# Kernel optimization log

Measured on AMD Instinct MI355X. Metric: run time of the kernel, lower is better.

Reference implementation:

```python
import jax, jax.numpy as jnp
import numpy as np

NUM_HEADS = 16
HIDDEN = 1024
HEAD_DIM = HIDDEN // NUM_HEADS


def setup_inputs() -> dict:
    key = jax.random.key(0)
    ks = jax.random.split(key, 8)
    B, S = 4, 1024
    scale = 0.02
    return {
        "hidden_states": jax.random.normal(ks[0], (B, S, HIDDEN), jnp.float32),
        "attention_mask": jnp.zeros((B, 1, 1, S), jnp.float32),
        "Wq": jax.random.normal(ks[1], (HIDDEN, HIDDEN), jnp.float32) * scale,
        "bq": jnp.zeros((HIDDEN,), jnp.float32),
        "Wk": jax.random.normal(ks[2], (HIDDEN, HIDDEN), jnp.float32) * scale,
        "bk": jnp.zeros((HIDDEN,), jnp.float32),
        "Wv": jax.random.normal(ks[3], (HIDDEN, HIDDEN), jnp.float32) * scale,
        "bv": jnp.zeros((HIDDEN,), jnp.float32),
    }


def _split_heads(x):
    # [B,S,H] -> [B,heads,S,head_dim]
    B, S, _ = x.shape
    return x.reshape(B, S, NUM_HEADS, HEAD_DIM).transpose(0, 2, 1, 3)


def reference(hidden_states, attention_mask, Wq, bq, Wk, bk, Wv, bv):
    # torch.nn.Linear convention: y = x @ W.T + b
    q = _split_heads(hidden_states @ Wq.T + bq)
    k = _split_heads(hidden_states @ Wk.T + bk)
    v = _split_heads(hidden_states @ Wv.T + bv)
    scores = jnp.einsum('bhqd,bhkd->bhqk', q, k) * (HEAD_DIM ** -0.5)
    scores = scores + attention_mask  # broadcast [B,1,1,S]
    probs = jax.nn.softmax(scores, axis=-1)
    context = jnp.einsum('bhqk,bhkd->bhqd', probs, v)  # [B,heads,S,head_dim]
    B, _, S, _ = context.shape
    return context.transpose(0, 2, 1, 3).reshape(B, S, HIDDEN)
```

## Files before the change

### kernel.cpp

```cpp
#include <hip/hip_runtime.h>
#include <hip/hip_bf16.h>
#include <stdint.h>

#define NH 16
#define HID 1024
#define HD 64
#define NB 4
#define SS 1024
#define MTOT (NB*SS)

typedef __attribute__((ext_vector_type(8))) short bf16x8;
typedef __attribute__((ext_vector_type(4))) float f32x4;
typedef __attribute__((ext_vector_type(16))) float f32x16;

#define LOG2E 1.44269504088896f

__device__ __forceinline__ unsigned short f2bf(float f) {
  union { float f; unsigned u; } v; v.f = f;
  unsigned u = v.u;
  return (unsigned short)((u + 0x7FFFu + ((u >> 16) & 1u)) >> 16);
}

__device__ __forceinline__ unsigned cvtpk(float lo, float hi) {
  unsigned r;
  asm("v_cvt_pk_bf16_f32 %0, %1, %2" : "=v"(r) : "v"(lo), "v"(hi));
  return r;
}

__device__ __forceinline__ void pl32swap(unsigned &a, unsigned &b) {
  asm("v_permlane32_swap_b32 %0, %1" : "+v"(a), "+v"(b));
}

__device__ __forceinline__ float exp2fast(float x) {
  float r;
  asm("v_exp_f32 %0, %1" : "=v"(r) : "v"(x));
  return r;
}

__device__ __forceinline__ void async16(void* lds, const void* g) {
  __builtin_amdgcn_global_load_lds(
      (const __attribute__((address_space(1))) unsigned*)g,
      (__attribute__((address_space(3))) unsigned*)lds, 16, 0, 0);
}

__global__ void cvt_all(const float4* __restrict__ X,
                        const float4* __restrict__ Wq,
                        const float4* __restrict__ Wk,
                        const float4* __restrict__ Wv,
                        ushort4* __restrict__ Xb,
                        ushort4* __restrict__ Wb) {
  int i = blockIdx.x * 256 + threadIdx.x;
  const float4* src; ushort4* dst; int idx;
  if (i < (MTOT * HID / 4)) {
    src = X; dst = Xb; idx = i;
  } else {
    int j = i - (MTOT * HID / 4);
    int sel = j >> 18;
    idx = j & 262143;
    src = (sel == 0) ? Wq : (sel == 1) ? Wk : Wv;
    dst = Wb + (size_t)sel * 262144;
  }
  float4 v = src[idx];
  ushort4 o;
  o.x = f2bf(v.x); o.y = f2bf(v.y); o.z = f2bf(v.z); o.w = f2bf(v.w);
  dst[idx] = o;
}

__global__ __launch_bounds__(256) void qkv_gemm(
    const ushort* __restrict__ Xb,
    const ushort* __restrict__ Wb,
    const float* __restrict__ bq,
    const float* __restrict__ bk,
    const float* __restrict__ bv,
    ushort* __restrict__ Q,
    ushort* __restrict__ K,
    ushort* __restrict__ Vt)
{
  __shared__ __attribute__((aligned(16))) ushort Al[3][128 * 32];
  __shared__ __attribute__((aligned(16))) ushort Bl[3][128 * 32];

  int bid = blockIdx.x;
  int swz = (bid & 7) * 96 + (bid >> 3);
  const int nbn = 3072 / 128;
  int bm = swz / nbn, bn = swz % nbn;
  int m0 = bm * 128, n0 = bn * 128;

  int tid = threadIdx.x;
  int wave = tid >> 6, lane = tid & 63;
  int g = lane >> 4, c = lane & 15;
  int wr = wave >> 1, wc = wave & 1;

  int srow = tid >> 2;
  int schunk = tid & 3;
  int ssw = (srow >> 1) & 3;
  const ushort* Asrc0 = Xb + (size_t)(m0 + srow) * 1024 + ((schunk ^ ssw) << 3);
  const ushort* Asrc1 = Xb + (size_t)(m0 + 64 + srow) * 1024 + ((schunk ^ ssw) << 3);
  const ushort* Bsrc0 = Wb + (size_t)(n0 + srow) * 1024 + ((schunk ^ ssw) << 3);
  const ushort* Bsrc1 = Wb + (size_t)(n0 + 64 + srow) * 1024 + ((schunk ^ ssw) << 3);
  int soff = srow * 64 + schunk * 16;

#define GSTAGE(bi) do {                                   \
    char* la_ = (char*)Al[bi]; char* lb_ = (char*)Bl[bi]; \
    async16(la_ + soff,        Asrc0);                    \
    async16(la_ + 4096 + soff, Asrc1);                    \
    async16(lb_ + soff,        Bsrc0);                    \
    async16(lb_ + 4096 + soff, Bsrc1);                    \
    Asrc0 += 32; Asrc1 += 32; Bsrc0 += 32; Bsrc1 += 32;   \
  } while (0)

  f32x4 acc[4][4] = {};
  int rsw = (c >> 1) & 3;
  int ch = ((g ^ rsw) << 4);

  GSTAGE(0);
  GSTAGE(1);

  int cur = 0, nxt = 2;
  for (int ks = 0; ks < 32; ++ks) {
    if (ks < 31) {
      asm volatile("s_waitcnt vmcnt(4)" ::: "memory");
    } else {
      asm volatile("s_waitcnt vmcnt(0)" ::: "memory");
    }
    __builtin_amdgcn_sched_barrier(0);
    __builtin_amdgcn_s_barrier();
    __builtin_amdgcn_sched_barrier(0);
    if (ks < 30) GSTAGE(nxt);

    const char* la = (const char*)Al[cur];
    const char* lb = (const char*)Bl[cur];
    bf16x8 a[4], b[4];
    #pragma unroll
    for (int m = 0; m < 4; ++m)
      a[m] = *(const bf16x8*)(la + (wr * 64 + m * 16 + c) * 64 + ch);
    #pragma unroll
    for (int n = 0; n < 4; ++n)
      b[n] = *(const bf16x8*)(lb + (wc * 64 + n * 16 + c) * 64 + ch);
    __builtin_amdgcn_s_setprio(1);
    #pragma unroll
    for (int m = 0; m < 4; ++m)
      #pragma unroll
      for (int n = 0; n < 4; ++n)
        acc[m][n] = __builtin_amdgcn_mfma_f32_16x16x32_bf16(a[m], b[n], acc[m][n], 0, 0, 0);
    __builtin_amdgcn_s_setprio(0);

    cur = (cur == 2) ? 0 : cur + 1;
    nxt = (nxt == 2) ? 0 : nxt + 1;
  }
#undef GSTAGE

  int sel = n0 >> 10;
  const float* bp = (sel == 0) ? bq : (sel == 1) ? bk : bv;
  float scl = (sel == 0) ? 0.125f * LOG2E : 1.0f;

  #pragma unroll
  for (int n = 0; n < 4; ++n) {
    int nn = (n0 & 1023) + wc * 64 + n * 16 + c;
    float bias = bp[nn];
    int h = nn >> 6, d = nn & 63;
    #pragma unroll
    for (int m = 0; m < 4; ++m) {
      int rowg = m0 + wr * 64 + m * 16 + g * 4;
      int bb = rowg >> 10;
      int s = rowg & 1023;
      #pragma unroll
      for (int r = 0; r < 4; ++r) {
        float val = (acc[m][n][r] + bias) * scl;
        unsigned short ob = f2bf(val);
        if (sel == 0)
          Q[(size_t)((bb * 16 + h) * 1024 + s + r) * 64 + d] = ob;
        else if (sel == 1)
          K[(size_t)((bb * 16 + h) * 1024 + s + r) * 64 + d] = ob;
        else
          Vt[(size_t)((bb * 16 + h) * 64 + d) * 1024 + s + r] = ob;
      }
    }
  }
}

__device__ __forceinline__ void build_pa(const f32x16& p, bf16x8& pa0, bf16x8& pa1) {
  unsigned W0 = cvtpk(p[0],  p[1]);
  unsigned W1 = cvtpk(p[2],  p[3]);
  unsigned W2 = cvtpk(p[4],  p[5]);
  unsigned W3 = cvtpk(p[6],  p[7]);
  unsigned W4 = cvtpk(p[8],  p[9]);
  unsigned W5 = cvtpk(p[10], p[11]);
  unsigned W6 = cvtpk(p[12], p[13]);
  unsigned W7 = cvtpk(p[14], p[15]);
  pl32swap(W0, W2);
  pl32swap(W1, W3);
  pl32swap(W4, W6);
  pl32swap(W5, W7);
  union { unsigned u[4]; bf16x8 v; } a0, a1;
  a0.u[0] = W0; a0.u[1] = W1; a0.u[2] = W2; a0.u[3] = W3;
  a1.u[0] = W4; a1.u[1] = W5; a1.u[2] = W6; a1.u[3] = W7;
  pa0 = a0.v; pa1 = a1.v;
}

__global__ __launch_bounds__(128) void attn(
    const ushort* __restrict__ Q,
    const ushort* __restrict__ K,
    const ushort* __restrict__ Vt,
    const float* __restrict__ mask,
    float* __restrict__ out)
{
  __shared__ __attribute__((aligned(16))) char kv_lds[2][16384];
  __shared__ float mask_s[SS];

  int blk = blockIdx.x;
  int xcd = blk & 7;
  int j = blk >> 3;
  int bh = xcd * 8 + (j >> 4);
  int qt = j & 15;
  int b = bh >> 4, h = bh & 15;
  int tid = threadIdx.x, wave = tid >> 6, lane = tid & 63;
  int r31 = lane & 31, hi = lane >> 5;
  int rsw = r31 & 7;
  int hib = hi << 4;
  int q0 = qt * 64 + wave * 32;

  const ushort* Qb = Q + (size_t)bh * SS * 64;
  const ushort* Kb = K + (size_t)bh * SS * 64;
  const ushort* Vb = Vt + (size_t)bh * 64 * SS;

  for (int i = tid; i < SS; i += 128) mask_s[i] = mask[b * SS + i] * LOG2E;

  bf16x8 qf[4];
  #pragma unroll
  for (int kp = 0; kp < 4; ++kp)
    qf[kp] = *(const bf16x8*)(Qb + (size_t)(q0 + r31) * 64 + kp * 16 + hi * 8);

  int srow = lane >> 3;
  int gck = (lane & 7) ^ srow;
  bool isK = (wave == 0);
  const ushort* sbase = isK
      ? (Kb + (size_t)srow * 64 + gck * 8)
      : (Vb + (size_t)srow * SS + gck * 8);
  const size_t sistep = isK ? (size_t)8 * 64 : (size_t)8 * SS;
  const int sadv = isK ? 64 * 64 : 64;
  int sldso = isK ? 0 : 8192;

#define STAGE(bufidx) do {                                  \
    char* lb_ = kv_lds[bufidx] + sldso;                     \
    _Pragma("unroll")                                       \
    for (int i_ = 0; i_ < 8; ++i_)                          \
      async16(lb_ + i_ * 1024 + lane * 16,                  \
              sbase + (size_t)i_ * sistep);                 \
    sbase += sadv;                                          \
  } while (0)

  STAGE(0);
  __syncthreads();

  f32x16 o0 = (f32x16)0.0f, o1 = (f32x16)0.0f;
  float mrow = 0.f, lrow = 0.f;

  int cur = 0;
  for (int it = 0; it < 16; ++it) {
    if (it < 15) STAGE(cur ^ 1);

    const char* kb0 = kv_lds[cur];
    const char* vb0 = kv_lds[cur] + 8192;

    f32x16 s0 = (f32x16)0.0f, s1 = (f32x16)0.0f;
    __builtin_amdgcn_s_setprio(1);
    #pragma unroll
    for (int kp = 0; kp < 4; ++kp) {
      int ch = (((kp << 1) | hi) ^ rsw) << 4;
      bf16x8 ka = *(const bf16x8*)(kb0 + r31 * 128 + ch);
      bf16x8 kc = *(const bf16x8*)(kb0 + (32 + r31) * 128 + ch);
      s0 = __builtin_amdgcn_mfma_f32_32x32x16_bf16(ka, qf[kp], s0, 0, 0, 0);
      s1 = __builtin_amdgcn_mfma_f32_32x32x16_bf16(kc, qf[kp], s1, 0, 0, 0);
    }
    __builtin_amdgcn_s_setprio(0);

    int kv = it * 64;
    #pragma unroll
    for (int sq = 0; sq < 4; ++sq) {
      f32x4 mk0 = *(const f32x4*)(&mask_s[kv + sq * 8 + hi * 4]);
      f32x4 mk1 = *(const f32x4*)(&mask_s[kv + 32 + sq * 8 + hi * 4]);
      #pragma unroll
      for (int r = 0; r < 4; ++r) {
        s0[sq * 4 + r] += mk0[r];
        s1[sq * 4 + r] += mk1[r];
      }
    }

    float mx = s0[0];
    #pragma unroll
    for (int i = 1; i < 16; ++i) mx = fmaxf(mx, s0[i]);
    #pragma unroll
    for (int i = 0; i < 16; ++i) mx = fmaxf(mx, s1[i]);
    mx = fmaxf(mx, __shfl_xor(mx, 32));

    if (!__all(mx <= mrow + 11.5416f)) {
      float mn = fmaxf(mrow, mx);
      float sc = exp2fast(mrow - mn);
      mrow = mn;
      lrow *= sc;
      #pragma unroll
      for (int i = 0; i < 16; ++i) {
        int qh = (i & 3) + 8 * (i >> 2);
        float scq = __uint_as_float((unsigned)__builtin_amdgcn_ds_bpermute(
            (qh << 2) + hib, (int)__float_as_uint(sc)));
        o0[i] *= scq; o1[i] *= scq;
      }
    }

    f32x16 p0, p1;
    float rs = 0.f;
    #pragma unroll
    for (int i = 0; i < 16; ++i) { float e = exp2fast(s0[i] - mrow); p0[i] = e; rs += e; }
    #pragma unroll
    for (int i = 0; i < 16; ++i) { float e = exp2fast(s1[i] - mrow); p1[i] = e; rs += e; }
    rs += __shfl_xor(rs, 32);
    lrow += rs;

    #pragma unroll
    for (int T = 0; T < 2; ++T) {
      bf16x8 pa0, pa1;
      build_pa(T ? p1 : p0, pa0, pa1);
      __builtin_amdgcn_s_setprio(1);
      #pragma unroll
      for (int kh = 0; kh < 2; ++kh) {
        int kap = 2 * T + kh;
        int ch = (((kap << 1) | hi) ^ rsw) << 4;
        bf16x8 va = *(const bf16x8*)(vb0 + r31 * 128 + ch);
        bf16x8 vc = *(const bf16x8*)(vb0 + (32 + r31) * 128 + ch);
        bf16x8 pf = kh ? pa1 : pa0;
        o0 = __builtin_amdgcn_mfma_f32_32x32x16_bf16(pf, va, o0, 0, 0, 0);
        o1 = __builtin_amdgcn_mfma_f32_32x32x16_bf16(pf, vc, o1, 0, 0, 0);
      }
      __builtin_amdgcn_s_setprio(0);
    }

    asm volatile("s_waitcnt vmcnt(0)" ::: "memory");
    __builtin_amdgcn_sched_barrier(0);
    __builtin_amdgcn_s_barrier();
    __builtin_amdgcn_sched_barrier(0);
    cur ^= 1;
  }
#undef STAGE

  float inv = 1.0f / lrow;
  #pragma unroll
  for (int i = 0; i < 16; ++i) {
    int qh = (i & 3) + 8 * (i >> 2);
    float li = __uint_as_float((unsigned)__builtin_amdgcn_ds_bpermute(
        (qh << 2) + hib, (int)__float_as_uint(inv)));
    int row = q0 + qh + 4 * hi;
    float* op = out + (size_t)(b * SS + row) * 1024 + h * 64 + r31;
    op[0]  = o0[i] * li;
    op[32] = o1[i] * li;
  }
}

extern "C" void kernel_launch(void* const* d_in, const int* in_sizes, int n_in,
                              void* d_out, int out_size, void* d_ws, size_t ws_size,
                              hipStream_t stream) {
  const float* hs   = (const float*)d_in[0];
  const float* mask = (const float*)d_in[1];
  const float* Wq   = (const float*)d_in[2];
  const float* bq   = (const float*)d_in[3];
  const float* Wk   = (const float*)d_in[4];
  const float* bk   = (const float*)d_in[5];
  const float* Wv   = (const float*)d_in[6];
  const float* bv   = (const float*)d_in[7];
  float* out = (float*)d_out;

  char* ws = (char*)d_ws;
  ushort* Xb = (ushort*)(ws);
  ushort* Wb = (ushort*)(ws + (8u  << 20));
  ushort* Qp = (ushort*)(ws + (14u << 20));
  ushort* Kp = (ushort*)(ws + (22u << 20));
  ushort* Vt = (ushort*)(ws + (30u << 20));

  cvt_all<<<7168, 256, 0, stream>>>((const float4*)hs, (const float4*)Wq,
                                    (const float4*)Wk, (const float4*)Wv,
                                    (ushort4*)Xb, (ushort4*)Wb);
  qkv_gemm<<<768, 256, 0, stream>>>(Xb, Wb, bq, bk, bv, Qp, Kp, Vt);
  attn<<<1024, 128, 0, stream>>>(Qp, Kp, Vt, mask, out);
}
```

Before: 88.16 us.

## Process two 32-row query tiles per wave to reuse K/V fragments

Each attention wave now handles 64 query rows, as two independent 32-row tiles with separate online-softmax state, instead of 32. The grid is halved to 512 blocks. K and V fragments are loaded from LDS once and fed to both tiles' MFMAs, which halves LDS reads and K/V staging per query row. The cost is much higher register pressure, managed with launch_bounds(128,2), and fewer blocks to spread across CUs.

```diff
diff --git a/kernel.cpp b/kernel.cpp
--- a/kernel.cpp
+++ b/kernel.cpp
@@ -197,7 +197,7 @@
   pa0 = a0.v; pa1 = a1.v;
 }
 
-__global__ __launch_bounds__(128) void attn(
+__global__ __launch_bounds__(128, 2) void attn(
     const ushort* __restrict__ Q,
     const ushort* __restrict__ K,
     const ushort* __restrict__ Vt,
@@ -210,14 +210,14 @@
   int blk = blockIdx.x;
   int xcd = blk & 7;
   int j = blk >> 3;
-  int bh = xcd * 8 + (j >> 4);
-  int qt = j & 15;
+  int bh = xcd * 8 + (j >> 3);
+  int qt = j & 7;
   int b = bh >> 4, h = bh & 15;
   int tid = threadIdx.x, wave = tid >> 6, lane = tid & 63;
   int r31 = lane & 31, hi = lane >> 5;
   int rsw = r31 & 7;
   int hib = hi << 4;
-  int q0 = qt * 64 + wave * 32;
+  int q0 = qt * 128 + wave * 64;
 
   const ushort* Qb = Q + (size_t)bh * SS * 64;
   const ushort* Kb = K + (size_t)bh * SS * 64;
@@ -225,10 +225,12 @@
 
   for (int i = tid; i < SS; i += 128) mask_s[i] = mask[b * SS + i] * LOG2E;
 
-  bf16x8 qf[4];
+  bf16x8 qfA[4], qfB[4];
   #pragma unroll
-  for (int kp = 0; kp < 4; ++kp)
-    qf[kp] = *(const bf16x8*)(Qb + (size_t)(q0 + r31) * 64 + kp * 16 + hi * 8);
+  for (int kp = 0; kp < 4; ++kp) {
+    qfA[kp] = *(const bf16x8*)(Qb + (size_t)(q0 + r31) * 64 + kp * 16 + hi * 8);
+    qfB[kp] = *(const bf16x8*)(Qb + (size_t)(q0 + 32 + r31) * 64 + kp * 16 + hi * 8);
+  }
 
   int srow = lane >> 3;
   int gck = (lane & 7) ^ srow;
@@ -252,8 +254,9 @@
   STAGE(0);
   __syncthreads();
 
-  f32x16 o0 = (f32x16)0.0f, o1 = (f32x16)0.0f;
-  float mrow = 0.f, lrow = 0.f;
+  f32x16 oA0 = (f32x16)0.0f, oA1 = (f32x16)0.0f;
+  f32x16 oB0 = (f32x16)0.0f, oB1 = (f32x16)0.0f;
+  float mrowA = 0.f, lrowA = 0.f, mrowB = 0.f, lrowB = 0.f;
 
   int cur = 0;
   for (int it = 0; it < 16; ++it) {
@@ -262,15 +265,22 @@
     const char* kb0 = kv_lds[cur];
     const char* vb0 = kv_lds[cur] + 8192;
 
-    f32x16 s0 = (f32x16)0.0f, s1 = (f32x16)0.0f;
-    __builtin_amdgcn_s_setprio(1);
+    bf16x8 ka[4], kc[4];
     #pragma unroll
     for (int kp = 0; kp < 4; ++kp) {
       int ch = (((kp << 1) | hi) ^ rsw) << 4;
-      bf16x8 ka = *(const bf16x8*)(kb0 + r31 * 128 + ch);
-      bf16x8 kc = *(const bf16x8*)(kb0 + (32 + r31) * 128 + ch);
-      s0 = __builtin_amdgcn_mfma_f32_32x32x16_bf16(ka, qf[kp], s0, 0, 0, 0);
-      s1 = __builtin_amdgcn_mfma_f32_32x32x16_bf16(kc, qf[kp], s1, 0, 0, 0);
+      ka[kp] = *(const bf16x8*)(kb0 + r31 * 128 + ch);
+      kc[kp] = *(const bf16x8*)(kb0 + (32 + r31) * 128 + ch);
+    }
+    f32x16 s0A = (f32x16)0.0f, s1A = (f32x16)0.0f;
+    f32x16 s0B = (f32x16)0.0f, s1B = (f32x16)0.0f;
+    __builtin_amdgcn_s_setprio(1);
+    #pragma unroll
+    for (int kp = 0; kp < 4; ++kp) {
+      s0A = __builtin_amdgcn_mfma_f32_32x32x16_bf16(ka[kp], qfA[kp], s0A, 0, 0, 0);
+      s1A = __builtin_amdgcn_mfma_f32_32x32x16_bf16(kc[kp], qfA[kp], s1A, 0, 0, 0);
+      s0B = __builtin_amdgcn_mfma_f32_32x32x16_bf16(ka[kp], qfB[kp], s0B, 0, 0, 0);
+      s1B = __builtin_amdgcn_mfma_f32_32x32x16_bf16(kc[kp], qfB[kp], s1B, 0, 0, 0);
     }
     __builtin_amdgcn_s_setprio(0);
 
@@ -281,55 +291,86 @@
       f32x4 mk1 = *(const f32x4*)(&mask_s[kv + 32 + sq * 8 + hi * 4]);
       #pragma unroll
       for (int r = 0; r < 4; ++r) {
-        s0[sq * 4 + r] += mk0[r];
-        s1[sq * 4 + r] += mk1[r];
+        s0A[sq * 4 + r] += mk0[r]; s1A[sq * 4 + r] += mk1[r];
+        s0B[sq * 4 + r] += mk0[r]; s1B[sq * 4 + r] += mk1[r];
       }
     }
 
-    float mx = s0[0];
-    #pragma unroll
-    for (int i = 1; i < 16; ++i) mx = fmaxf(mx, s0[i]);
-    #pragma unroll
-    for (int i = 0; i < 16; ++i) mx = fmaxf(mx, s1[i]);
-    mx = fmaxf(mx, __shfl_xor(mx, 32));
-
-    if (!__all(mx <= mrow + 11.5416f)) {
-      float mn = fmaxf(mrow, mx);
-      float sc = exp2fast(mrow - mn);
-      mrow = mn;
-      lrow *= sc;
+    float mxA = s0A[0];
+    #pragma unroll
+    for (int i = 1; i < 16; ++i) mxA = fmaxf(mxA, s0A[i]);
+    #pragma unroll
+    for (int i = 0; i < 16; ++i) mxA = fmaxf(mxA, s1A[i]);
+    mxA = fmaxf(mxA, __shfl_xor(mxA, 32));
+    if (!__all(mxA <= mrowA + 11.5416f)) {
+      float mn = fmaxf(mrowA, mxA);
+      float sc = exp2fast(mrowA - mn);
+      mrowA = mn; lrowA *= sc;
       #pragma unroll
       for (int i = 0; i < 16; ++i) {
         int qh = (i & 3) + 8 * (i >> 2);
         float scq = __uint_as_float((unsigned)__builtin_amdgcn_ds_bpermute(
             (qh << 2) + hib, (int)__float_as_uint(sc)));
-        o0[i] *= scq; o1[i] *= scq;
+        oA0[i] *= scq; oA1[i] *= scq;
       }
     }
-
-    f32x16 p0, p1;
-    float rs = 0.f;
-    #pragma unroll
-    for (int i = 0; i < 16; ++i) { float e = exp2fast(s0[i] - mrow); p0[i] = e; rs += e; }
-    #pragma unroll
-    for (int i = 0; i < 16; ++i) { float e = exp2fast(s1[i] - mrow); p1[i] = e; rs += e; }
-    rs += __shfl_xor(rs, 32);
-    lrow += rs;
+    float rsA = 0.f;
+    #pragma unroll
+    for (int i = 0; i < 16; ++i) { float e = exp2fast(s0A[i] - mrowA); s0A[i] = e; rsA += e; }
+    #pragma unroll
+    for (int i = 0; i < 16; ++i) { float e = exp2fast(s1A[i] - mrowA); s1A[i] = e; rsA += e; }
+    rsA += __shfl_xor(rsA, 32);
+    lrowA += rsA;
+
+    float mxB = s0B[0];
+    #pragma unroll
+    for (int i = 1; i < 16; ++i) mxB = fmaxf(mxB, s0B[i]);
+    #pragma unroll
+    for (int i = 0; i < 16; ++i) mxB = fmaxf(mxB, s1B[i]);
+    mxB = fmaxf(mxB, __shfl_xor(mxB, 32));
+    if (!__all(mxB <= mrowB + 11.5416f)) {
+      float mn = fmaxf(mrowB, mxB);
+      float sc = exp2fast(mrowB - mn);
+      mrowB = mn; lrowB *= sc;
+      #pragma unroll
+      for (int i = 0; i < 16; ++i) {
+        int qh = (i & 3) + 8 * (i >> 2);
+        float scq = __uint_as_float((unsigned)__builtin_amdgcn_ds_bpermute(
+            (qh << 2) + hib, (int)__float_as_uint(sc)));
+        oB0[i] *= scq; oB1[i] *= scq;
+      }
+    }
+    float rsB = 0.f;
+    #pragma unroll
+    for (int i = 0; i < 16; ++i) { float e = exp2fast(s0B[i] - mrowB); s0B[i] = e; rsB += e; }
+    #pragma unroll
+    for (int i = 0; i < 16; ++i) { float e = exp2fast(s1B[i] - mrowB); s1B[i] = e; rsB += e; }
+    rsB += __shfl_xor(rsB, 32);
+    lrowB += rsB;
+
+    bf16x8 va[4], vc[4];
+    #pragma unroll
+    for (int kap = 0; kap < 4; ++kap) {
+      int ch = (((kap << 1) | hi) ^ rsw) << 4;
+      va[kap] = *(const bf16x8*)(vb0 + r31 * 128 + ch);
+      vc[kap] = *(const bf16x8*)(vb0 + (32 + r31) * 128 + ch);
+    }
 
     #pragma unroll
     for (int T = 0; T < 2; ++T) {
-      bf16x8 pa0, pa1;
-      build_pa(T ? p1 : p0, pa0, pa1);
+      bf16x8 paA0, paA1, paB0, paB1;
+      build_pa(T ? s1A : s0A, paA0, paA1);
+      build_pa(T ? s1B : s0B, paB0, paB1);
       __builtin_amdgcn_s_setprio(1);
       #pragma unroll
       for (int kh = 0; kh < 2; ++kh) {
         int kap = 2 * T + kh;
-        int ch = (((kap << 1) | hi) ^ rsw) << 4;
-        bf16x8 va = *(const bf16x8*)(vb0 + r31 * 128 + ch);
-        bf16x8 vc = *(const bf16x8*)(vb0 + (32 + r31) * 128 + ch);
-        bf16x8 pf = kh ? pa1 : pa0;
-        o0 = __builtin_amdgcn_mfma_f32_32x32x16_bf16(pf, va, o0, 0, 0, 0);
-        o1 = __builtin_amdgcn_mfma_f32_32x32x16_bf16(pf, vc, o1, 0, 0, 0);
+        bf16x8 pfA = kh ? paA1 : paA0;
+        bf16x8 pfB = kh ? paB1 : paB0;
+        oA0 = __builtin_amdgcn_mfma_f32_32x32x16_bf16(pfA, va[kap], oA0, 0, 0, 0);
+        oA1 = __builtin_amdgcn_mfma_f32_32x32x16_bf16(pfA, vc[kap], oA1, 0, 0, 0);
+        oB0 = __builtin_amdgcn_mfma_f32_32x32x16_bf16(pfB, va[kap], oB0, 0, 0, 0);
+        oB1 = __builtin_amdgcn_mfma_f32_32x32x16_bf16(pfB, vc[kap], oB1, 0, 0, 0);
       }
       __builtin_amdgcn_s_setprio(0);
     }
@@ -342,16 +383,21 @@
   }
 #undef STAGE
 
-  float inv = 1.0f / lrow;
+  float invA = 1.0f / lrowA, invB = 1.0f / lrowB;
   #pragma unroll
   for (int i = 0; i < 16; ++i) {
     int qh = (i & 3) + 8 * (i >> 2);
-    float li = __uint_as_float((unsigned)__builtin_amdgcn_ds_bpermute(
-        (qh << 2) + hib, (int)__float_as_uint(inv)));
-    int row = q0 + qh + 4 * hi;
-    float* op = out + (size_t)(b * SS + row) * 1024 + h * 64 + r31;
-    op[0]  = o0[i] * li;
-    op[32] = o1[i] * li;
+    float liA = __uint_as_float((unsigned)__builtin_amdgcn_ds_bpermute(
+        (qh << 2) + hib, (int)__float_as_uint(invA)));
+    float liB = __uint_as_float((unsigned)__builtin_amdgcn_ds_bpermute(
+        (qh << 2) + hib, (int)__float_as_uint(invB)));
+    int rowA = q0 + qh + 4 * hi;
+    float* opA = out + (size_t)(b * SS + rowA) * 1024 + h * 64 + r31;
+    opA[0]  = oA0[i] * liA;
+    opA[32] = oA1[i] * liA;
+    float* opB = out + (size_t)(b * SS + rowA + 32) * 1024 + h * 64 + r31;
+    opB[0]  = oB0[i] * liB;
+    opB[32] = oB1[i] * liB;
   }
 }
 
@@ -379,5 +425,5 @@
                                     (const float4*)Wk, (const float4*)Wv,
                                     (ushort4*)Xb, (ushort4*)Wb);
   qkv_gemm<<<768, 256, 0, stream>>>(Xb, Wb, bq, bk, bv, Qp, Kp, Vt);
-  attn<<<1024, 128, 0, stream>>>(Qp, Kp, Vt, mask, out);
-}
+  attn<<<512, 128, 0, stream>>>(Qp, Kp, Vt, mask, out);
+}
```

Measured after the change: 101.1 us. 14.7% more time.
